# Kernel tuning notes

Hardware: AMD Instinct MI355X
Metric: run time of the kernel (lower is better)

## Reference

```python
import jax, jax.numpy as jnp
import numpy as np

N_HEAD = 16
N_FEAT = 1024
D_K = N_FEAT // N_HEAD


def setup_inputs() -> dict:
    key = jax.random.key(0)
    ks = jax.random.split(key, 11)
    B, T1, T2 = 2, 2048, 2048
    s = 0.02
    return {
        "query": jax.random.normal(ks[0], (B, T1, N_FEAT), jnp.float32),
        "key_": jax.random.normal(ks[1], (B, T2, N_FEAT), jnp.float32),
        "value": jax.random.normal(ks[2], (B, T2, N_FEAT), jnp.float32),
        "mask": jnp.ones((B, T1, T2), jnp.int32),
        "Wq": jax.random.normal(ks[3], (N_FEAT, N_FEAT), jnp.float32) * s,
        "bq": jnp.zeros((N_FEAT,), jnp.float32),
        "Wk": jax.random.normal(ks[4], (N_FEAT, N_FEAT), jnp.float32) * s,
        "bk": jnp.zeros((N_FEAT,), jnp.float32),
        "Wv": jax.random.normal(ks[5], (N_FEAT, N_FEAT), jnp.float32) * s,
        "bv": jnp.zeros((N_FEAT,), jnp.float32),
        "Wo": jax.random.normal(ks[6], (N_FEAT, N_FEAT), jnp.float32) * s,
        "bo": jnp.zeros((N_FEAT,), jnp.float32),
    }


def reference(query, key_, value, mask, Wq, bq, Wk, bk, Wv, bv, Wo, bo):
    B = query.shape[0]
    # project and split heads: (B, T, F) -> (B, H, T, d_k)
    def heads(x, W, b):
        y = x @ W + b
        return y.reshape(B, -1, N_HEAD, D_K).transpose(0, 2, 1, 3)

    q = heads(query, Wq, bq)
    k = heads(key_, Wk, bk)
    v = heads(value, Wv, bv)

    scale = jnp.sqrt(jnp.asarray(D_K, jnp.float32))
    scores = jnp.einsum("bhqd,bhkd->bhqk", q, k) / scale  # (B,H,T1,T2)
    m = mask[:, None, :, :]  # (B,1,T1,T2)
    scores = jnp.where(m > 0, scores, jnp.asarray(-10000.0, scores.dtype))
    attn = jax.nn.softmax(scores, axis=-1)
    # dropout_rate = 0.0 / inference -> identity
    x = jnp.einsum("bhqk,bhkd->bhqd", attn, v)
    x = x.transpose(0, 2, 1, 3).reshape(B, -1, N_FEAT)
    return x @ Wo + bo
```

## Files before the change

kernel.cpp:

```cpp
#include <hip/hip_runtime.h>
#include <hip/hip_bf16.h>
#include <stdint.h>

typedef float  f32x4 __attribute__((ext_vector_type(4)));
typedef short  s16x8 __attribute__((ext_vector_type(8)));
typedef short  s16x4 __attribute__((ext_vector_type(4)));
typedef int    i32x4 __attribute__((ext_vector_type(4)));

#define DI __device__ __forceinline__

constexpr int Bb = 2, Tt = 2048, Ff = 1024, Hh = 16, Dk = 64;
constexpr int Mm = Bb * Tt;
constexpr float LOG2E = 1.44269504088896340736f;

DI ushort f2bf(float f) {
  unsigned u = __float_as_uint(f);
  unsigned r = (u + 0x7fffu + ((u >> 16) & 1u)) >> 16;
  return (ushort)r;
}

DI int cvt_pk_bf16(float lo, float hi) {
  __hip_bfloat162 t = __float22bfloat162_rn(make_float2(lo, hi));
  int w;
  __builtin_memcpy(&w, &t, 4);
  return w;
}

DI void gload16(const void* g, void* l) {
  __builtin_amdgcn_global_load_lds(
      (__attribute__((address_space(1))) void*)g,
      (__attribute__((address_space(3))) void*)l, 16, 0, 0);
}

DI void wait_vm4() { asm volatile("s_waitcnt vmcnt(4)" ::: "memory"); }
DI void wait_vm0() { asm volatile("s_waitcnt vmcnt(0)" ::: "memory"); }

__global__ __launch_bounds__(256) void cvt3_kernel(const float* __restrict__ s0, const float* __restrict__ s1,
                                                   const float* __restrict__ s2, ushort* __restrict__ d0,
                                                   ushort* __restrict__ d1, ushort* __restrict__ d2, int n8) {
  const float* src = blockIdx.y == 0 ? s0 : (blockIdx.y == 1 ? s1 : s2);
  ushort* dst = blockIdx.y == 0 ? d0 : (blockIdx.y == 1 ? d1 : d2);
  int i = blockIdx.x * 256 + threadIdx.x;
  if (i >= n8) return;
  const float4* s4 = (const float4*)src + (size_t)i * 2;
  float4 a = s4[0], b = s4[1];
  s16x8 o;
  o[0] = (short)f2bf(a.x); o[1] = (short)f2bf(a.y); o[2] = (short)f2bf(a.z); o[3] = (short)f2bf(a.w);
  o[4] = (short)f2bf(b.x); o[5] = (short)f2bf(b.y); o[6] = (short)f2bf(b.z); o[7] = (short)f2bf(b.w);
  *((s16x8*)dst + i) = o;
}

__global__ __launch_bounds__(256) void wtrans_kernel(const float* __restrict__ W0, const float* __restrict__ W1,
                                                     const float* __restrict__ W2, const float* __restrict__ W3,
                                                     ushort* __restrict__ Wt0, ushort* __restrict__ Wt1,
                                                     ushort* __restrict__ Wt2, ushort* __restrict__ Wt3) {
  const float* W; ushort* Wt;
  switch (blockIdx.z) {
    case 0: W = W0; Wt = Wt0; break;
    case 1: W = W1; Wt = Wt1; break;
    case 2: W = W2; Wt = Wt2; break;
    default: W = W3; Wt = Wt3; break;
  }
  __shared__ float tile[64][65];
  int k0 = blockIdx.y * 64, n0 = blockIdx.x * 64;
  int t = threadIdx.x, r = t >> 4, c4 = (t & 15) * 4;
#pragma unroll
  for (int i = 0; i < 4; i++) {
    int row = r + i * 16;
    const float4 v = *(const float4*)(W + (size_t)(k0 + row) * Ff + n0 + c4);
    tile[row][c4] = v.x; tile[row][c4 + 1] = v.y; tile[row][c4 + 2] = v.z; tile[row][c4 + 3] = v.w;
  }
  __syncthreads();
#pragma unroll
  for (int i = 0; i < 4; i++) {
    int n = r + i * 16;
    s16x4 o;
#pragma unroll
    for (int j = 0; j < 4; j++) o[j] = (short)f2bf(tile[c4 + j][n]);
    *(s16x4*)(Wt + (size_t)(n0 + n) * Ff + k0 + c4) = o;
  }
}

__global__ __launch_bounds__(256) void maskflag_kernel(const int* __restrict__ mask, int* __restrict__ flags) {
  int kb = blockIdx.x, qb = blockIdx.y, b = blockIdx.z;
  int t = threadIdx.x;
  __shared__ int s;
  if (t == 0) s = 1;
  __syncthreads();
  int ok = 1;
#pragma unroll
  for (int i = 0; i < 4; i++) {
    int row = qb * 64 + (t >> 4) + i * 16;
    const int4 v = *(const int4*)(mask + ((size_t)b * Tt + row) * Tt + kb * 64 + (t & 15) * 4);
    ok &= (v.x > 0) & (v.y > 0) & (v.z > 0) & (v.w > 0);
  }
  atomicAnd(&s, ok);
  __syncthreads();
  if (t == 0) flags[(b * 32 + qb) * 32 + kb] = s;
}

DI void gemm_core(const ushort* __restrict__ A, const ushort* __restrict__ Bt,
                  const float* __restrict__ bias, void* __restrict__ Cout, float scale, int mode,
                  int m0, int n0) {
  __shared__ ushort Ads[3][128 * 32];
  __shared__ ushort Bds[3][128 * 32];
  const int tid = threadIdx.x, lane = tid & 63, w = tid >> 6;
  const int wr = w >> 1, wc = w & 1;
  const int g = lane >> 4, ln = lane & 15;
  const int strow = tid >> 2;
  const int stc = (tid & 3) * 8;

  const ushort* Asrc0 = A + (size_t)(m0 + strow) * Ff + stc;
  const ushort* Asrc1 = A + (size_t)(m0 + 64 + strow) * Ff + stc;
  const ushort* Bsrc0 = Bt + (size_t)(n0 + strow) * Ff + stc;
  const ushort* Bsrc1 = Bt + (size_t)(n0 + 64 + strow) * Ff + stc;
  const int dst0 = strow * 32 + stc;
  const int dst1 = (64 + strow) * 32 + stc;

  f32x4 acc[4][4];
#pragma unroll
  for (int m = 0; m < 4; m++)
#pragma unroll
    for (int n = 0; n < 4; n++) acc[m][n] = (f32x4){0.f, 0.f, 0.f, 0.f};

  auto stage = [&](int t, int slot) {
    const int k0 = t * 32;
    gload16(Asrc0 + k0, Ads[slot] + dst0);
    gload16(Asrc1 + k0, Ads[slot] + dst1);
    gload16(Bsrc0 + k0, Bds[slot] + dst0);
    gload16(Bsrc1 + k0, Bds[slot] + dst1);
  };

  stage(0, 0);
  stage(1, 1);

  int rs = 0, ws = 2;
  for (int t = 0; t < 32; ++t) {
    if (t < 31) wait_vm4(); else wait_vm0();
    __builtin_amdgcn_s_barrier();
    __builtin_amdgcn_sched_barrier(0);
    if (t < 30) stage(t + 2, ws);
    const ushort* As = Ads[rs];
    const ushort* Bs = Bds[rs];
    s16x8 af[4], bf[4];
#pragma unroll
    for (int m = 0; m < 4; m++) af[m] = *(const s16x8*)(As + (wr * 64 + m * 16 + ln) * 32 + g * 8);
#pragma unroll
    for (int n = 0; n < 4; n++) bf[n] = *(const s16x8*)(Bs + (wc * 64 + n * 16 + ln) * 32 + g * 8);
    __builtin_amdgcn_s_setprio(1);
#pragma unroll
    for (int m = 0; m < 4; m++)
#pragma unroll
      for (int n = 0; n < 4; n++)
        acc[m][n] = __builtin_amdgcn_mfma_f32_16x16x32_bf16(af[m], bf[n], acc[m][n], 0, 0, 0);
    __builtin_amdgcn_s_setprio(0);
    rs = rs == 2 ? 0 : rs + 1;
    ws = ws == 2 ? 0 : ws + 1;
  }
#pragma unroll
  for (int m = 0; m < 4; m++) {
    const int r0 = m0 + wr * 64 + m * 16 + g * 4;
#pragma unroll
    for (int n = 0; n < 4; n++) {
      const int col = n0 + wc * 64 + n * 16 + ln;
      const float bv = bias[col];
      if (mode == 2) {
        const int bb = r0 >> 11, rb = r0 & 2047;
        const int x = rb & 63;
        const int pbase = (x & 0x20) | ((x & 0x0C) << 1) | ((x & 0x10) >> 2);
        s16x4 o4;
#pragma unroll
        for (int r = 0; r < 4; r++) o4[r] = (short)f2bf(acc[m][n][r] + bv);
        *(s16x4*)((ushort*)Cout + ((size_t)bb * Ff + col) * Tt + (rb & ~63) + pbase) = o4;
      } else {
#pragma unroll
        for (int r = 0; r < 4; r++) {
          const float val = (acc[m][n][r] + bv) * scale;
          if (mode == 1)
            ((ushort*)Cout)[(size_t)(r0 + r) * Ff + col] = f2bf(val);
          else
            ((float*)Cout)[(size_t)(r0 + r) * Ff + col] = val;
        }
      }
    }
  }
}

__global__ __launch_bounds__(256) void qkv_gemm_kernel(
    const ushort* __restrict__ Xq, const ushort* __restrict__ Xk, const ushort* __restrict__ Xv,
    const ushort* __restrict__ Wqt, const ushort* __restrict__ Wkt, const ushort* __restrict__ Wvt,
    const float* __restrict__ bq, const float* __restrict__ bk, const float* __restrict__ bv,
    ushort* __restrict__ Qb, ushort* __restrict__ Kb, ushort* __restrict__ Vpt) {
  const int lin = blockIdx.x + 8 * blockIdx.y + 256 * blockIdx.z;
  const int work = (lin & 7) * 96 + (lin >> 3);
  const int z = work >> 8;
  const int r = work & 255;
  const int m0 = (r >> 3) * 128, n0 = (r & 7) * 128;
  const ushort* A = z == 0 ? Xq : (z == 1 ? Xk : Xv);
  const ushort* Wt = z == 0 ? Wqt : (z == 1 ? Wkt : Wvt);
  const float* bias = z == 0 ? bq : (z == 1 ? bk : bv);
  void* C = z == 0 ? (void*)Qb : (z == 1 ? (void*)Kb : (void*)Vpt);
  const float scale = z == 0 ? 0.125f * LOG2E : 1.0f;
  gemm_core(A, Wt, bias, C, scale, z == 2 ? 2 : 1, m0, n0);
}

__global__ __launch_bounds__(256) void out_gemm_kernel(const ushort* __restrict__ AO,
                                                       const ushort* __restrict__ Wot,
                                                       const float* __restrict__ bo,
                                                       float* __restrict__ Out) {
  const int lin = blockIdx.x + 8 * blockIdx.y;
  const int work = (lin & 7) * 32 + (lin >> 3);
  const int m0 = (work >> 3) * 128, n0 = (work & 7) * 128;
  gemm_core(AO, Wot, bo, Out, 1.0f, 0, m0, n0);
}

__global__ __launch_bounds__(256) void flash_kernel(
    const ushort* __restrict__ Qb, const ushort* __restrict__ Kb, const ushort* __restrict__ Vpt,
    const int* __restrict__ flags, const int* __restrict__ mask, ushort* __restrict__ AO) {
  __shared__ ushort Ks[3][64 * 64];
  __shared__ ushort Vs[3][64 * 64];
  const int lin = blockIdx.x + 16 * (blockIdx.y + 16 * blockIdx.z);
  const int work = (lin & 7) * 64 + (lin >> 3);
  const int qb = work & 15, h = (work >> 4) & 15, b = work >> 8;
  const int tid = threadIdx.x, lane = tid & 63, w = tid >> 6;
  const int g = lane >> 4, ln = lane & 15;

  const ushort* Qg = Qb + ((size_t)b * Tt + qb * 128) * Ff + h * Dk;
  const ushort* Kg = Kb + ((size_t)b * Tt) * Ff + h * Dk;
  const ushort* Vg = Vpt + (size_t)(b * Ff + h * Dk) * Tt;

  const int srow = lane >> 3;
  const int swzch = ((lane & 7) ^ srow) * 8;

  s16x8 qf0[2], qf1[2];
  {
    const ushort* Qrow0 = Qg + (size_t)(w * 16 + ln) * Ff;
    const ushort* Qrow1 = Qrow0 + (size_t)64 * Ff;
    qf0[0] = *(const s16x8*)(Qrow0 + g * 8);
    qf0[1] = *(const s16x8*)(Qrow0 + 32 + g * 8);
    qf1[0] = *(const s16x8*)(Qrow1 + g * 8);
    qf1[1] = *(const s16x8*)(Qrow1 + 32 + g * 8);
  }
  const int* flagrow0 = flags + (b * 32 + qb * 2) * 32;
  const int f0 = (lane < 32) ? flagrow0[lane] : 1;
  const int f1 = (lane < 32) ? flagrow0[32 + lane] : 1;

  auto stage = [&](int t, int slot) {
    const ushort* Kg2 = Kg + (size_t)t * 64 * Ff;
    const ushort* Vg2 = Vg + (size_t)t * 64;
#pragma unroll
    for (int it = 0; it < 2; ++it) {
      const int row = w * 16 + it * 8;
      gload16(Kg2 + (size_t)(row + srow) * Ff + swzch, Ks[slot] + row * 64);
      gload16(Vg2 + (size_t)(row + srow) * Tt + swzch, Vs[slot] + row * 64);
    }
  };
  stage(0, 0);
  stage(1, 1);
  const unsigned long long bm0 = __ballot(f0 == 0);
  const unsigned long long bm1 = __ballot(f1 == 0);

  float l0 = 0.f, l1 = 0.f;
  f32x4 o0[4], o1[4];
#pragma unroll
  for (int ds = 0; ds < 4; ds++) { o0[ds] = (f32x4){0.f, 0.f, 0.f, 0.f}; o1[ds] = (f32x4){0.f, 0.f, 0.f, 0.f}; }

  int rs = 0, ws = 2;
  for (int kt = 0; kt < 32; ++kt) {
    if (kt < 31) wait_vm4(); else wait_vm0();
    __builtin_amdgcn_s_barrier();
    __builtin_amdgcn_sched_barrier(0);
    if (kt < 30) stage(kt + 2, ws);
    const ushort* Kc = Ks[rs];
    const ushort* Vc = Vs[rs];
    f32x4 sf0[4], sf1[4];
    __builtin_amdgcn_s_setprio(1);
#pragma unroll
    for (int ks = 0; ks < 4; ++ks) {
      f32x4 a0 = (f32x4){0.f, 0.f, 0.f, 0.f};
      f32x4 a1 = (f32x4){0.f, 0.f, 0.f, 0.f};
#pragma unroll
      for (int c = 0; c < 2; c++) {
        const int row = ks * 16 + ln;
        const int off = (c * 64 + g * 16) ^ ((row & 7) << 4);
        const s16x8 kf = *(const s16x8*)((const char*)Kc + row * 128 + off);
        a0 = __builtin_amdgcn_mfma_f32_16x16x32_bf16(kf, qf0[c], a0, 0, 0, 0);
        a1 = __builtin_amdgcn_mfma_f32_16x16x32_bf16(kf, qf1[c], a1, 0, 0, 0);
      }
      sf0[ks] = a0; sf1[ks] = a1;
    }
    __builtin_amdgcn_s_setprio(0);
    if ((bm0 >> kt) & 1ull) {
      const int qg_ = qb * 128 + w * 16 + ln;
#pragma unroll
      for (int ks = 0; ks < 4; ++ks) {
        const int4 mv = *(const int4*)(mask + ((size_t)b * Tt + qg_) * Tt + kt * 64 + ks * 16 + g * 4);
        if (mv.x <= 0) sf0[ks][0] = -10000.f;
        if (mv.y <= 0) sf0[ks][1] = -10000.f;
        if (mv.z <= 0) sf0[ks][2] = -10000.f;
        if (mv.w <= 0) sf0[ks][3] = -10000.f;
      }
    }
    if ((bm1 >> kt) & 1ull) {
      const int qg_ = qb * 128 + 64 + w * 16 + ln;
#pragma unroll
      for (int ks = 0; ks < 4; ++ks) {
        const int4 mv = *(const int4*)(mask + ((size_t)b * Tt + qg_) * Tt + kt * 64 + ks * 16 + g * 4);
        if (mv.x <= 0) sf1[ks][0] = -10000.f;
        if (mv.y <= 0) sf1[ks][1] = -10000.f;
        if (mv.z <= 0) sf1[ks][2] = -10000.f;
        if (mv.w <= 0) sf1[ks][3] = -10000.f;
      }
    }
    float a0 = 0.f, a1 = 0.f;
#pragma unroll
    for (int ks = 0; ks < 4; ++ks) {
#pragma unroll
      for (int r = 0; r < 4; ++r) {
        const float p0 = __builtin_amdgcn_exp2f(sf0[ks][r]);
        const float p1 = __builtin_amdgcn_exp2f(sf1[ks][r]);
        sf0[ks][r] = p0; sf1[ks][r] = p1;
        a0 += p0; a1 += p1;
      }
    }
    l0 += a0; l1 += a1;
    i32x4 paw0[2], paw1[2];
#pragma unroll
    for (int c = 0; c < 2; c++)
#pragma unroll
      for (int f = 0; f < 2; f++)
#pragma unroll
        for (int hh = 0; hh < 2; hh++) {
          paw0[c][f * 2 + hh] = cvt_pk_bf16(sf0[2 * c + f][2 * hh], sf0[2 * c + f][2 * hh + 1]);
          paw1[c][f * 2 + hh] = cvt_pk_bf16(sf1[2 * c + f][2 * hh], sf1[2 * c + f][2 * hh + 1]);
        }
    const s16x8 pa00 = __builtin_bit_cast(s16x8, paw0[0]);
    const s16x8 pa01 = __builtin_bit_cast(s16x8, paw0[1]);
    const s16x8 pa10 = __builtin_bit_cast(s16x8, paw1[0]);
    const s16x8 pa11 = __builtin_bit_cast(s16x8, paw1[1]);
    __builtin_amdgcn_s_setprio(1);
#pragma unroll
    for (int ds = 0; ds < 4; ++ds) {
      const int row = ds * 16 + ln;
#pragma unroll
      for (int c = 0; c < 2; ++c) {
        const int off = (c * 64 + g * 16) ^ ((row & 7) << 4);
        const s16x8 vf = *(const s16x8*)((const char*)Vc + row * 128 + off);
        o0[ds] = __builtin_amdgcn_mfma_f32_16x16x32_bf16(c == 0 ? pa00 : pa01, vf, o0[ds], 0, 0, 0);
        o1[ds] = __builtin_amdgcn_mfma_f32_16x16x32_bf16(c == 0 ? pa10 : pa11, vf, o1[ds], 0, 0, 0);
      }
    }
    __builtin_amdgcn_s_setprio(0);
    rs = rs == 2 ? 0 : rs + 1;
    ws = ws == 2 ? 0 : ws + 1;
  }

  l0 += __shfl_xor(l0, 16); l0 += __shfl_xor(l0, 32);
  l1 += __shfl_xor(l1, 16); l1 += __shfl_xor(l1, 32);
  float inv0[4], inv1[4];
#pragma unroll
  for (int r = 0; r < 4; ++r) {
    inv0[r] = 1.0f / __shfl(l0, g * 4 + r);
    inv1[r] = 1.0f / __shfl(l1, g * 4 + r);
  }
  ushort* AOg0 = AO + ((size_t)b * Tt + qb * 128 + w * 16) * Ff + h * Dk;
  ushort* AOg1 = AOg0 + (size_t)64 * Ff;
#pragma unroll
  for (int ds = 0; ds < 4; ++ds)
#pragma unroll
    for (int r = 0; r < 4; ++r) {
      AOg0[(size_t)(g * 4 + r) * Ff + ds * 16 + ln] = f2bf(o0[ds][r] * inv0[r]);
      AOg1[(size_t)(g * 4 + r) * Ff + ds * 16 + ln] = f2bf(o1[ds][r] * inv1[r]);
    }
}

extern "C" void kernel_launch(void* const* d_in, const int* in_sizes, int n_in,
                              void* d_out, int out_size, void* d_ws, size_t ws_size,
                              hipStream_t stream) {
  const float* query = (const float*)d_in[0];
  const float* key_  = (const float*)d_in[1];
  const float* value = (const float*)d_in[2];
  const int*   mask  = (const int*)d_in[3];
  const float* Wq = (const float*)d_in[4];  const float* bq = (const float*)d_in[5];
  const float* Wk = (const float*)d_in[6];  const float* bk = (const float*)d_in[7];
  const float* Wv = (const float*)d_in[8];  const float* bv = (const float*)d_in[9];
  const float* Wo = (const float*)d_in[10]; const float* bo = (const float*)d_in[11];
  float* Out = (float*)d_out;

  constexpr size_t SZ_X = (size_t)Mm * Ff * 2;
  constexpr size_t SZ_W = (size_t)Ff * Ff * 2;
  uintptr_t p = (uintptr_t)d_ws;
  auto alloc = [&](size_t sz) { void* r = (void*)p; p += (sz + 255) & ~(size_t)255; return r; };
  ushort* Xq = (ushort*)alloc(SZ_X);
  ushort* Xk = (ushort*)alloc(SZ_X);
  ushort* Xv = (ushort*)alloc(SZ_X);
  ushort* Wqt = (ushort*)alloc(SZ_W);
  ushort* Wkt = (ushort*)alloc(SZ_W);
  ushort* Wvt = (ushort*)alloc(SZ_W);
  ushort* Wot = (ushort*)alloc(SZ_W);
  ushort* Qp  = (ushort*)alloc(SZ_X);
  ushort* Kp  = (ushort*)alloc(SZ_X);
  ushort* Vpt = (ushort*)alloc(SZ_X);
  int* flags = (int*)alloc((size_t)Bb * 32 * 32 * 4);
  ushort* AO = Xq;

  const int n8 = Mm * Ff / 8;
  cvt3_kernel<<<dim3(2048, 3), 256, 0, stream>>>(query, key_, value, Xq, Xk, Xv, n8);
  wtrans_kernel<<<dim3(16, 16, 4), 256, 0, stream>>>(Wq, Wk, Wv, Wo, Wqt, Wkt, Wvt, Wot);
  maskflag_kernel<<<dim3(32, 32, 2), 256, 0, stream>>>(mask, flags);
  qkv_gemm_kernel<<<dim3(8, 32, 3), 256, 0, stream>>>(Xq, Xk, Xv, Wqt, Wkt, Wvt, bq, bk, bv, Qp, Kp, Vpt);
  flash_kernel<<<dim3(16, 16, 2), 256, 0, stream>>>(Qp, Kp, Vpt, flags, mask, AO);
  out_gemm_kernel<<<dim3(8, 32), 256, 0, stream>>>(AO, Wot, bo, Out);
}
```

Baseline: 144.0 us.

## Split flash attention over two key halves and merge partials in a combine kernel

The flash kernel now processes only half of the key/value tiles per block, doubling the grid. Each block writes unnormalised bf16 partial outputs and row sums. A new combine kernel adds the two halves and divides by the summed denominators. The staging pipeline also drops from three LDS buffers to two, with a full sync per tile. The aim is more resident blocks per CU for better latency hiding, at the cost of an extra pass over the attention output and some precision loss from storing bf16 partials.

```diff
diff --git a/kernel.cpp b/kernel.cpp
--- a/kernel.cpp
+++ b/kernel.cpp
@@ -18,6 +18,8 @@
   unsigned r = (u + 0x7fffu + ((u >> 16) & 1u)) >> 16;
   return (ushort)r;
 }
+
+DI float b2f(ushort u) { return __uint_as_float((unsigned)u << 16); }
 
 DI int cvt_pk_bf16(float lo, float hi) {
   __hip_bfloat162 t = __float22bfloat162_rn(make_float2(lo, hi));
@@ -216,12 +218,15 @@
 
 __global__ __launch_bounds__(256) void flash_kernel(
     const ushort* __restrict__ Qb, const ushort* __restrict__ Kb, const ushort* __restrict__ Vpt,
-    const int* __restrict__ flags, const int* __restrict__ mask, ushort* __restrict__ AO) {
-  __shared__ ushort Ks[3][64 * 64];
-  __shared__ ushort Vs[3][64 * 64];
+    const int* __restrict__ flags, const int* __restrict__ mask,
+    ushort* __restrict__ Opart, float* __restrict__ Lpart) {
+  __shared__ ushort Ks[2][64 * 64];
+  __shared__ ushort Vs[2][64 * 64];
   const int lin = blockIdx.x + 16 * (blockIdx.y + 16 * blockIdx.z);
-  const int work = (lin & 7) * 64 + (lin >> 3);
-  const int qb = work & 15, h = (work >> 4) & 15, b = work >> 8;
+  const int work = (lin & 7) * 128 + (lin >> 3);
+  const int qb = work & 15, h = (work >> 4) & 15, rest = work >> 8;
+  const int b = rest >> 1, half = rest & 1;
+  const int kt0 = half * 16;
   const int tid = threadIdx.x, lane = tid & 63, w = tid >> 6;
   const int g = lane >> 4, ln = lane & 15;
 
@@ -245,18 +250,13 @@
   const int f0 = (lane < 32) ? flagrow0[lane] : 1;
   const int f1 = (lane < 32) ? flagrow0[32 + lane] : 1;
 
-  auto stage = [&](int t, int slot) {
-    const ushort* Kg2 = Kg + (size_t)t * 64 * Ff;
-    const ushort* Vg2 = Vg + (size_t)t * 64;
-#pragma unroll
-    for (int it = 0; it < 2; ++it) {
-      const int row = w * 16 + it * 8;
-      gload16(Kg2 + (size_t)(row + srow) * Ff + swzch, Ks[slot] + row * 64);
-      gload16(Vg2 + (size_t)(row + srow) * Tt + swzch, Vs[slot] + row * 64);
-    }
-  };
-  stage(0, 0);
-  stage(1, 1);
+#pragma unroll
+  for (int it = 0; it < 2; ++it) {
+    const int row = w * 16 + it * 8;
+    gload16(Kg + (size_t)(kt0 * 64 + row + srow) * Ff + swzch, Ks[0] + row * 64);
+    gload16(Vg + (size_t)(row + srow) * Tt + kt0 * 64 + swzch, Vs[0] + row * 64);
+  }
+  __syncthreads();
   const unsigned long long bm0 = __ballot(f0 == 0);
   const unsigned long long bm1 = __ballot(f1 == 0);
 
@@ -265,14 +265,17 @@
 #pragma unroll
   for (int ds = 0; ds < 4; ds++) { o0[ds] = (f32x4){0.f, 0.f, 0.f, 0.f}; o1[ds] = (f32x4){0.f, 0.f, 0.f, 0.f}; }
 
-  int rs = 0, ws = 2;
-  for (int kt = 0; kt < 32; ++kt) {
-    if (kt < 31) wait_vm4(); else wait_vm0();
-    __builtin_amdgcn_s_barrier();
-    __builtin_amdgcn_sched_barrier(0);
-    if (kt < 30) stage(kt + 2, ws);
-    const ushort* Kc = Ks[rs];
-    const ushort* Vc = Vs[rs];
+  auto body = [&](const ushort* Kc, const ushort* Vc, ushort* Kn, ushort* Vn, int kt) {
+    if (kt + 1 < kt0 + 16) {
+      const ushort* Kg2 = Kg + (size_t)(kt + 1) * 64 * Ff;
+      const ushort* Vg2 = Vg + (size_t)(kt + 1) * 64;
+#pragma unroll
+      for (int it = 0; it < 2; ++it) {
+        const int row = w * 16 + it * 8;
+        gload16(Kg2 + (size_t)(row + srow) * Ff + swzch, Kn + row * 64);
+        gload16(Vg2 + (size_t)(row + srow) * Tt + swzch, Vn + row * 64);
+      }
+    }
     f32x4 sf0[4], sf1[4];
     __builtin_amdgcn_s_setprio(1);
 #pragma unroll
@@ -351,27 +354,50 @@
       }
     }
     __builtin_amdgcn_s_setprio(0);
-    rs = rs == 2 ? 0 : rs + 1;
-    ws = ws == 2 ? 0 : ws + 1;
+    __syncthreads();
+  };
+
+  for (int kt = kt0; kt < kt0 + 16; kt += 2) {
+    body(Ks[0], Vs[0], Ks[1], Vs[1], kt);
+    body(Ks[1], Vs[1], Ks[0], Vs[0], kt + 1);
   }
 
   l0 += __shfl_xor(l0, 16); l0 += __shfl_xor(l0, 32);
   l1 += __shfl_xor(l1, 16); l1 += __shfl_xor(l1, 32);
-  float inv0[4], inv1[4];
-#pragma unroll
-  for (int r = 0; r < 4; ++r) {
-    inv0[r] = 1.0f / __shfl(l0, g * 4 + r);
-    inv1[r] = 1.0f / __shfl(l1, g * 4 + r);
-  }
-  ushort* AOg0 = AO + ((size_t)b * Tt + qb * 128 + w * 16) * Ff + h * Dk;
-  ushort* AOg1 = AOg0 + (size_t)64 * Ff;
+  if (lane < 16) {
+    const int qg0 = qb * 128 + w * 16 + lane;
+    Lpart[(((size_t)(half * 2 + b) * Tt) + qg0) * Hh + h] = l0;
+    Lpart[(((size_t)(half * 2 + b) * Tt) + qg0 + 64) * Hh + h] = l1;
+  }
+  ushort* Og0 = Opart + (((size_t)half * Mm + b * Tt + qb * 128 + w * 16) << 10) + h * Dk;
+  ushort* Og1 = Og0 + ((size_t)64 << 10);
 #pragma unroll
   for (int ds = 0; ds < 4; ++ds)
 #pragma unroll
     for (int r = 0; r < 4; ++r) {
-      AOg0[(size_t)(g * 4 + r) * Ff + ds * 16 + ln] = f2bf(o0[ds][r] * inv0[r]);
-      AOg1[(size_t)(g * 4 + r) * Ff + ds * 16 + ln] = f2bf(o1[ds][r] * inv1[r]);
-    }
+      Og0[(size_t)(g * 4 + r) * Ff + ds * 16 + ln] = f2bf(o0[ds][r]);
+      Og1[(size_t)(g * 4 + r) * Ff + ds * 16 + ln] = f2bf(o1[ds][r]);
+    }
+}
+
+__global__ __launch_bounds__(256) void combine_kernel(const ushort* __restrict__ Opart,
+                                                      const float* __restrict__ Lpart,
+                                                      ushort* __restrict__ AO) {
+  const int i = blockIdx.x * 256 + threadIdx.x;
+  const size_t e = (size_t)i * 8;
+  const int row = (int)(e >> 10);
+  const int col = (int)(e & 1023);
+  const int h = col >> 6;
+  const int b = row >> 11, q = row & 2047;
+  const float l = Lpart[(((size_t)b * Tt) + q) * Hh + h] +
+                  Lpart[(((size_t)(2 + b) * Tt) + q) * Hh + h];
+  const float rcp = 1.0f / l;
+  const s16x8 a = *(const s16x8*)(Opart + e);
+  const s16x8 c = *(const s16x8*)(Opart + ((size_t)Mm << 10) + e);
+  s16x8 o;
+#pragma unroll
+  for (int j = 0; j < 8; ++j) o[j] = (short)f2bf((b2f((ushort)a[j]) + b2f((ushort)c[j])) * rcp);
+  *(s16x8*)(AO + e) = o;
 }
 
 extern "C" void kernel_launch(void* const* d_in, const int* in_sizes, int n_in,
@@ -402,6 +428,8 @@
   ushort* Kp  = (ushort*)alloc(SZ_X);
   ushort* Vpt = (ushort*)alloc(SZ_X);
   int* flags = (int*)alloc((size_t)Bb * 32 * 32 * 4);
+  float* Lpart = (float*)alloc((size_t)2 * Bb * Tt * Hh * 4);
+  ushort* Opart = Xk;
   ushort* AO = Xq;
 
   const int n8 = Mm * Ff / 8;
@@ -409,6 +437,7 @@
   wtrans_kernel<<<dim3(16, 16, 4), 256, 0, stream>>>(Wq, Wk, Wv, Wo, Wqt, Wkt, Wvt, Wot);
   maskflag_kernel<<<dim3(32, 32, 2), 256, 0, stream>>>(mask, flags);
   qkv_gemm_kernel<<<dim3(8, 32, 3), 256, 0, stream>>>(Xq, Xk, Xv, Wqt, Wkt, Wvt, bq, bk, bv, Qp, Kp, Vpt);
-  flash_kernel<<<dim3(16, 16, 2), 256, 0, stream>>>(Qp, Kp, Vpt, flags, mask, AO);
+  flash_kernel<<<dim3(16, 16, 4), 256, 0, stream>>>(Qp, Kp, Vpt, flags, mask, Opart, Lpart);
+  combine_kernel<<<dim3(2048), 256, 0, stream>>>(Opart, Lpart, AO);
   out_gemm_kernel<<<dim3(8, 32), 256, 0, stream>>>(AO, Wot, bo, Out);
 }
```

New measurement: 145.1 us. No clear change (+0.7%).

## Switch flash K/V staging to double buffering with unrolled buffer select

Applied to the files above, without the earlier changes.

Replaces the three-slot K/V LDS ring with two slots, which cuts shared memory per block and may allow more resident blocks. The loop is unrolled by two so the buffer index is a compile-time constant, and a __syncthreads at the end of each step replaces the vmcnt wait plus barrier. Swizzled LDS read offsets are precomputed once, and the softmax row sums are accumulated as vectors. In exchange the prefetch distance drops from two tiles to one, so global-load latency is less hidden, and the full sync drains all outstanding loads every step.

```diff
diff --git a/kernel.cpp b/kernel.cpp
--- a/kernel.cpp
+++ b/kernel.cpp
@@ -217,8 +217,8 @@
 __global__ __launch_bounds__(256) void flash_kernel(
     const ushort* __restrict__ Qb, const ushort* __restrict__ Kb, const ushort* __restrict__ Vpt,
     const int* __restrict__ flags, const int* __restrict__ mask, ushort* __restrict__ AO) {
-  __shared__ ushort Ks[3][64 * 64];
-  __shared__ ushort Vs[3][64 * 64];
+  __shared__ ushort Ks[2][64 * 64];
+  __shared__ ushort Vs[2][64 * 64];
   const int lin = blockIdx.x + 16 * (blockIdx.y + 16 * blockIdx.z);
   const int work = (lin & 7) * 64 + (lin >> 3);
   const int qb = work & 15, h = (work >> 4) & 15, b = work >> 8;
@@ -231,6 +231,11 @@
 
   const int srow = lane >> 3;
   const int swzch = ((lane & 7) ^ srow) * 8;
+
+  const ushort* ksrc0 = Kg + (size_t)(w * 16 + srow) * Ff + swzch;
+  const ushort* ksrc1 = ksrc0 + (size_t)8 * Ff;
+  const ushort* vsrc0 = Vg + (size_t)(w * 16 + srow) * Tt + swzch;
+  const ushort* vsrc1 = vsrc0 + (size_t)8 * Tt;
 
   s16x8 qf0[2], qf1[2];
   {
@@ -245,34 +250,49 @@
   const int f0 = (lane < 32) ? flagrow0[lane] : 1;
   const int f1 = (lane < 32) ? flagrow0[32 + lane] : 1;
 
-  auto stage = [&](int t, int slot) {
-    const ushort* Kg2 = Kg + (size_t)t * 64 * Ff;
-    const ushort* Vg2 = Vg + (size_t)t * 64;
-#pragma unroll
-    for (int it = 0; it < 2; ++it) {
-      const int row = w * 16 + it * 8;
-      gload16(Kg2 + (size_t)(row + srow) * Ff + swzch, Ks[slot] + row * 64);
-      gload16(Vg2 + (size_t)(row + srow) * Tt + swzch, Vs[slot] + row * 64);
-    }
-  };
-  stage(0, 0);
-  stage(1, 1);
+  {
+    const int r0 = w * 16;
+    gload16(ksrc0, Ks[0] + r0 * 64);
+    gload16(ksrc1, Ks[0] + (r0 + 8) * 64);
+    gload16(vsrc0, Vs[0] + r0 * 64);
+    gload16(vsrc1, Vs[0] + (r0 + 8) * 64);
+    ksrc0 += (size_t)64 * Ff; ksrc1 += (size_t)64 * Ff;
+    vsrc0 += 64; vsrc1 += 64;
+  }
+  __syncthreads();
   const unsigned long long bm0 = __ballot(f0 == 0);
   const unsigned long long bm1 = __ballot(f1 == 0);
 
-  float l0 = 0.f, l1 = 0.f;
+  int loff[4][2];
+#pragma unroll
+  for (int i = 0; i < 4; i++)
+#pragma unroll
+    for (int c = 0; c < 2; c++) {
+      const int row = i * 16 + ln;
+      loff[i][c] = row * 128 + ((c * 64 + g * 16) ^ ((row & 7) << 4));
+    }
+  const char* Kbase = (const char*)&Ks[0][0];
+  const char* Vbase = (const char*)&Vs[0][0];
+
+  f32x4 l0v = (f32x4){0.f, 0.f, 0.f, 0.f}, l1v = (f32x4){0.f, 0.f, 0.f, 0.f};
   f32x4 o0[4], o1[4];
 #pragma unroll
   for (int ds = 0; ds < 4; ds++) { o0[ds] = (f32x4){0.f, 0.f, 0.f, 0.f}; o1[ds] = (f32x4){0.f, 0.f, 0.f, 0.f}; }
 
-  int rs = 0, ws = 2;
-  for (int kt = 0; kt < 32; ++kt) {
-    if (kt < 31) wait_vm4(); else wait_vm0();
-    __builtin_amdgcn_s_barrier();
-    __builtin_amdgcn_sched_barrier(0);
-    if (kt < 30) stage(kt + 2, ws);
-    const ushort* Kc = Ks[rs];
-    const ushort* Vc = Vs[rs];
+  auto body = [&](int bsel, int kt) {
+    if (kt + 1 < 32) {
+      ushort* Kn = Ks[bsel ^ 1];
+      ushort* Vn = Vs[bsel ^ 1];
+      const int r0 = w * 16;
+      gload16(ksrc0, Kn + r0 * 64);
+      gload16(ksrc1, Kn + (r0 + 8) * 64);
+      gload16(vsrc0, Vn + r0 * 64);
+      gload16(vsrc1, Vn + (r0 + 8) * 64);
+      ksrc0 += (size_t)64 * Ff; ksrc1 += (size_t)64 * Ff;
+      vsrc0 += 64; vsrc1 += 64;
+    }
+    const char* Kc = Kbase + bsel * 8192;
+    const char* Vc = Vbase + bsel * 8192;
     f32x4 sf0[4], sf1[4];
     __builtin_amdgcn_s_setprio(1);
 #pragma unroll
@@ -281,9 +301,7 @@
       f32x4 a1 = (f32x4){0.f, 0.f, 0.f, 0.f};
 #pragma unroll
       for (int c = 0; c < 2; c++) {
-        const int row = ks * 16 + ln;
-        const int off = (c * 64 + g * 16) ^ ((row & 7) << 4);
-        const s16x8 kf = *(const s16x8*)((const char*)Kc + row * 128 + off);
+        const s16x8 kf = *(const s16x8*)(Kc + loff[ks][c]);
         a0 = __builtin_amdgcn_mfma_f32_16x16x32_bf16(kf, qf0[c], a0, 0, 0, 0);
         a1 = __builtin_amdgcn_mfma_f32_16x16x32_bf16(kf, qf1[c], a1, 0, 0, 0);
       }
@@ -312,18 +330,16 @@
         if (mv.w <= 0) sf1[ks][3] = -10000.f;
       }
     }
-    float a0 = 0.f, a1 = 0.f;
 #pragma unroll
     for (int ks = 0; ks < 4; ++ks) {
 #pragma unroll
       for (int r = 0; r < 4; ++r) {
-        const float p0 = __builtin_amdgcn_exp2f(sf0[ks][r]);
-        const float p1 = __builtin_amdgcn_exp2f(sf1[ks][r]);
-        sf0[ks][r] = p0; sf1[ks][r] = p1;
-        a0 += p0; a1 += p1;
-      }
-    }
-    l0 += a0; l1 += a1;
+        sf0[ks][r] = __builtin_amdgcn_exp2f(sf0[ks][r]);
+        sf1[ks][r] = __builtin_amdgcn_exp2f(sf1[ks][r]);
+      }
+    }
+    l0v += sf0[0] + sf0[1] + sf0[2] + sf0[3];
+    l1v += sf1[0] + sf1[1] + sf1[2] + sf1[3];
     i32x4 paw0[2], paw1[2];
 #pragma unroll
     for (int c = 0; c < 2; c++)
@@ -341,20 +357,24 @@
     __builtin_amdgcn_s_setprio(1);
 #pragma unroll
     for (int ds = 0; ds < 4; ++ds) {
-      const int row = ds * 16 + ln;
 #pragma unroll
       for (int c = 0; c < 2; ++c) {
-        const int off = (c * 64 + g * 16) ^ ((row & 7) << 4);
-        const s16x8 vf = *(const s16x8*)((const char*)Vc + row * 128 + off);
+        const s16x8 vf = *(const s16x8*)(Vc + loff[ds][c]);
         o0[ds] = __builtin_amdgcn_mfma_f32_16x16x32_bf16(c == 0 ? pa00 : pa01, vf, o0[ds], 0, 0, 0);
         o1[ds] = __builtin_amdgcn_mfma_f32_16x16x32_bf16(c == 0 ? pa10 : pa11, vf, o1[ds], 0, 0, 0);
       }
     }
     __builtin_amdgcn_s_setprio(0);
-    rs = rs == 2 ? 0 : rs + 1;
-    ws = ws == 2 ? 0 : ws + 1;
-  }
-
+    __syncthreads();
+  };
+
+  for (int kt = 0; kt < 32; kt += 2) {
+    body(0, kt);
+    body(1, kt + 1);
+  }
+
+  float l0 = (l0v[0] + l0v[1]) + (l0v[2] + l0v[3]);
+  float l1 = (l1v[0] + l1v[1]) + (l1v[2] + l1v[3]);
   l0 += __shfl_xor(l0, 16); l0 += __shfl_xor(l0, 32);
   l1 += __shfl_xor(l1, 16); l1 += __shfl_xor(l1, 32);
   float inv0[4], inv1[4];
```

Result: faster. 137.9 us (-4.2%).
